# Kernel tuning notes

Measured on AMD Instinct MI355X. Metric: run time of the kernel, lower is better.

## Reference

```python
import jax, jax.numpy as jnp
import numpy as np

NUM_HEAD = 16

def _make_rope(max_len, dim_head, theta=10000.0):
    inv_freq = 1.0 / (theta ** (np.arange(0, dim_head, 2, dtype=np.float32) / dim_head))
    t = np.arange(max_len, dtype=np.float32)
    freqs = np.outer(t, inv_freq)  # [S, dim_head/2]
    return jnp.asarray(np.cos(freqs)), jnp.asarray(np.sin(freqs))

def setup_inputs() -> dict:
    key = jax.random.key(0)
    k1, k2, k3 = jax.random.split(key, 3)
    B, S, D = 2, 2048, 1024
    num_layer = 12
    std = 0.02 / np.sqrt(2 * num_layer)
    x = jax.random.normal(k1, (B, S, D), dtype=jnp.float32)
    wQKV = jax.random.normal(k2, (3 * D, D), dtype=jnp.float32) * std
    wOut = jax.random.normal(k3, (D, D), dtype=jnp.float32) * 0.02
    cos, sin = _make_rope(S, D // NUM_HEAD)
    return {"x": x, "wQKV": wQKV, "wOut": wOut, "cos": cos, "sin": sin}

def _apply_rope(t, cos, sin):
    # t: [B, H, S, dh]; cos/sin: [S, dh/2] -> broadcast [1,1,S,dh/2]
    te, to = t[..., ::2], t[..., 1::2]
    re = te * cos - to * sin
    ro = to * cos + te * sin
    return jnp.stack([re, ro], axis=-1).reshape(t.shape)

def reference(x, wQKV, wOut, cos, sin):
    B, S, D = x.shape
    H = NUM_HEAD
    dh = D // H
    qkv = x @ wQKV.T  # [B, S, 3D]
    q, k, v = jnp.split(qkv, 3, axis=-1)
    q = q.reshape(B, S, H, dh).transpose(0, 2, 1, 3)  # [B,H,S,dh]
    k = k.reshape(B, S, H, dh).transpose(0, 2, 1, 3)
    v = v.reshape(B, S, H, dh).transpose(0, 2, 1, 3)
    c = cos[:S][None, None]
    s = sin[:S][None, None]
    q = _apply_rope(q, c, s)
    k = _apply_rope(k, c, s)
    scores = jnp.einsum('bhsd,bhtd->bhst', q, k) / jnp.sqrt(jnp.asarray(dh, x.dtype))
    causal = jnp.tril(jnp.ones((S, S), dtype=bool))
    scores = jnp.where(causal, scores, jnp.asarray(-jnp.inf, scores.dtype))
    w = jax.nn.softmax(scores, axis=-1)
    out = jnp.einsum('bhst,bhtd->bhsd', w, v)  # [B,H,S,dh]
    out = out.transpose(0, 2, 1, 3).reshape(B, S, D)
    return out @ wOut.T
```

## Files before the change

kernel.cpp:

```cpp
#include <hip/hip_runtime.h>
#include <hip/hip_bf16.h>

typedef __attribute__((ext_vector_type(8))) short bf16x8;
typedef __attribute__((ext_vector_type(4))) short s16x4;
typedef __attribute__((ext_vector_type(4))) float f32x4;

__device__ __forceinline__ short f2bf(float f) {
    unsigned int u = __builtin_bit_cast(unsigned int, f);
    u += 0x7fffu + ((u >> 16) & 1u);
    return (short)(u >> 16);
}

#define GLDS(g, l) __builtin_amdgcn_global_load_lds( \
    (__attribute__((address_space(1))) void*)(g),    \
    (__attribute__((address_space(3))) void*)(l), 16, 0, 0)

#define BARSB() { __builtin_amdgcn_s_barrier(); __builtin_amdgcn_sched_barrier(0); }
#define VMC8()  { asm volatile("s_waitcnt vmcnt(8)" ::: "memory"); __builtin_amdgcn_sched_barrier(0); }
#define VMC7()  { asm volatile("s_waitcnt vmcnt(7)" ::: "memory"); __builtin_amdgcn_sched_barrier(0); }
#define VMC0()  { asm volatile("s_waitcnt vmcnt(0)" ::: "memory"); __builtin_amdgcn_sched_barrier(0); }

__global__ __launch_bounds__(256) void cvt_fused(const float* __restrict__ x,
                                                 const float* __restrict__ wq,
                                                 const float* __restrict__ wo,
                                                 const float* __restrict__ cosT,
                                                 const float* __restrict__ sinT,
                                                 short* __restrict__ xb,
                                                 short* __restrict__ wqb,
                                                 short* __restrict__ wob,
                                                 float2* __restrict__ csT) {
    const int b = blockIdx.x;
    if (b >= 8192) {
        const int idx = (b - 8192) * 256 + threadIdx.x;
        const int i2 = idx >> 11;
        const int s = idx & 2047;
        csT[idx] = make_float2(cosT[s * 32 + i2], sinT[s * 32 + i2]);
        return;
    }
    const float* in; short* out; int i;
    if (b < 4096)      { in = x;  out = xb;  i = b * 256 + threadIdx.x; }
    else if (b < 7168) { in = wq; out = wqb; i = (b - 4096) * 256 + threadIdx.x; }
    else               { in = wo; out = wob; i = (b - 7168) * 256 + threadIdx.x; }
    float4 v = reinterpret_cast<const float4*>(in)[i];
    s16x4 r = { f2bf(v.x), f2bf(v.y), f2bf(v.z), f2bf(v.w) };
    reinterpret_cast<s16x4*>(out)[i] = r;
}

#define LDP 72

__device__ __forceinline__ void load_a(const short* __restrict__ A, int wr, int lo, int hi,
                                       int mh, bf16x8 aF[4][2]) {
#pragma unroll
    for (int mi = 0; mi < 4; ++mi)
#pragma unroll
        for (int kk = 0; kk < 2; ++kk)
            aF[mi][kk] = *reinterpret_cast<const bf16x8*>(
                &A[(wr * 128 + mh * 64 + mi * 16 + lo) * 64 + (((kk * 4 + hi) ^ (lo & 7)) << 3)]);
}
__device__ __forceinline__ void load_b3(const short* __restrict__ B, int wc, int lo, int hi,
                                        bf16x8 bF[3][2]) {
#pragma unroll
    for (int ni = 0; ni < 3; ++ni)
#pragma unroll
        for (int kk = 0; kk < 2; ++kk)
            bF[ni][kk] = *reinterpret_cast<const bf16x8*>(
                &B[(wc * 48 + ni * 16 + lo) * 64 + (((kk * 4 + hi) ^ (lo & 7)) << 3)]);
}
__device__ __forceinline__ void mfma24(const bf16x8 aF[4][2], const bf16x8 bF[3][2],
                                       f32x4 acc[8][3], int mh) {
#pragma unroll
    for (int mi = 0; mi < 4; ++mi)
#pragma unroll
        for (int ni = 0; ni < 3; ++ni)
#pragma unroll
            for (int kk = 0; kk < 2; ++kk)
                acc[mh * 4 + mi][ni] = __builtin_amdgcn_mfma_f32_16x16x32_bf16(
                    aF[mi][kk], bF[ni][kk], acc[mh * 4 + mi][ni], 0, 0, 0);
}

__global__ __launch_bounds__(512, 1) void gemm_qkv_rope(
    const short* __restrict__ X, const short* __restrict__ W,
    const float2* __restrict__ csT,
    short* __restrict__ Qo, short* __restrict__ Ko, short* __restrict__ Vo) {
    __shared__ short ldsA[2][16384];
    __shared__ short ldsB[2][12288];
    const int tid = threadIdx.x;
    const int lane = tid & 63;
    const int w = tid >> 6;
    const int lo = lane & 15, hi = lane >> 4;
    const int wr = w >> 2, wc = w & 3;
    const int lin = blockIdx.x;
    const int xcd = lin & 7;
    const int i_ = lin >> 3;
    const int m0 = ((xcd >> 1) * 4 + (i_ & 3)) * 256;
    const int n0 = ((xcd & 1) * 8 + (i_ >> 2)) * 192;

    f32x4 acc[8][3];
#pragma unroll
    for (int i = 0; i < 8; i++)
#pragma unroll
        for (int j = 0; j < 3; j++) acc[i][j] = {0.f, 0.f, 0.f, 0.f};

    const int srow8 = w * 8 + (lane >> 3);
    const int scx = (((lane & 7) ^ ((lane >> 3) & 7)) << 3);

#define STAGE_A(BUF, KT, IT) GLDS(X + (size_t)(m0 + (IT) * 64 + srow8) * 1024 + ((KT) << 6) + scx, \
                                  (char*)&ldsA[BUF][0] + (IT) * 8192 + w * 1024)
#define STAGE_B(BUF, KT, IT) GLDS(W + (size_t)(n0 + (IT) * 64 + srow8) * 1024 + ((KT) << 6) + scx, \
                                  (char*)&ldsB[BUF][0] + (IT) * 8192 + w * 1024)

    bf16x8 aF[4][2], bF[3][2];

    STAGE_B(0, 0, 0); STAGE_B(0, 0, 1); STAGE_B(0, 0, 2);
    STAGE_A(0, 0, 0); STAGE_A(0, 0, 1); STAGE_A(0, 0, 2); STAGE_A(0, 0, 3);

    for (int t = 0; t < 16; ++t) {
        const int c = t & 1;
        if (t < 15) {
            const int nb_ = c ^ 1, t1 = t + 1;
            STAGE_B(nb_, t1, 0); STAGE_B(nb_, t1, 1); STAGE_B(nb_, t1, 2);
            STAGE_A(nb_, t1, 0); STAGE_A(nb_, t1, 1); STAGE_A(nb_, t1, 2); STAGE_A(nb_, t1, 3);
            VMC7();
        } else {
            VMC0();
        }
        BARSB();
        load_a(&ldsA[c][0], wr, lo, hi, 0, aF);
        load_b3(&ldsB[c][0], wc, lo, hi, bF);
        mfma24(aF, bF, acc, 0);
        load_a(&ldsA[c][0], wr, lo, hi, 1, aF);
        mfma24(aF, bF, acc, 1);
        if (t < 15) BARSB();
    }
#undef STAGE_A
#undef STAGE_B

    const int sfull = m0 + wr * 128 + (hi << 2);
    const int b_ = sfull >> 11;
    const int srow_ = sfull & 2047;
#pragma unroll
    for (int ni = 0; ni < 3; ni++) {
        const int n = n0 + wc * 48 + ni * 16 + lo;
        const int region = n >> 10;
        const int c = n & 1023;
        const int h = c >> 6;
        const int d = c & 63;
        const size_t obase = ((size_t)(b_ * 16 + h) * 2048 + srow_) * 64 + d;
        if (region == 2) {
#pragma unroll
            for (int mi = 0; mi < 8; mi++)
#pragma unroll
                for (int r = 0; r < 4; r++)
                    Vo[obase + (size_t)(mi * 16 + r) * 64] = f2bf(acc[mi][ni][r]);
        } else {
            short* dst = (region == 0) ? Qo : Ko;
            const float scale = (region == 0) ? 0.18033688f : 1.0f;
            const float2* csrow = csT + (size_t)(d >> 1) * 2048 + srow_;
#pragma unroll
            for (int mi = 0; mi < 8; mi++) {
                float4 t0 = *reinterpret_cast<const float4*>(csrow + mi * 16);
                float4 t1 = *reinterpret_cast<const float4*>(csrow + mi * 16 + 2);
                const float cs_[4] = {t0.x, t0.z, t1.x, t1.z};
                const float sn_[4] = {t0.y, t0.w, t1.y, t1.w};
#pragma unroll
                for (int r = 0; r < 4; r++) {
                    float v = acc[mi][ni][r];
                    float other = __shfl_xor(v, 1, 64);
                    float outv = (d & 1) ? (v * cs_[r] + other * sn_[r])
                                         : (v * cs_[r] - other * sn_[r]);
                    dst[obase + (size_t)(mi * 16 + r) * 64] = f2bf(outv * scale);
                }
            }
        }
    }
}

__device__ __forceinline__ void attn_tile_compute(
    const bf16x8 q0, const bf16x8 q1,
    const short* __restrict__ Ks,
    const short (*Vts)[LDP], short* __restrict__ Pw,
    const int lane, const int w, const bool diag,
    float& m_r, float& l_r, f32x4* __restrict__ o_acc) {
    const int lo = lane & 15, hi = lane >> 4;
    const int sx = lo & 7;

    f32x4 sc[4];
#pragma unroll
    for (int nb = 0; nb < 4; nb++) sc[nb] = {0.f, 0.f, 0.f, 0.f};
#pragma unroll
    for (int nb = 0; nb < 4; nb++) {
        const short* kr = &Ks[(nb * 16 + lo) * 64];
        bf16x8 k0 = *reinterpret_cast<const bf16x8*>(&kr[(hi ^ sx) << 3]);
        sc[nb] = __builtin_amdgcn_mfma_f32_16x16x32_bf16(k0, q0, sc[nb], 0, 0, 0);
        bf16x8 k1 = *reinterpret_cast<const bf16x8*>(&kr[((4 + hi) ^ sx) << 3]);
        sc[nb] = __builtin_amdgcn_mfma_f32_16x16x32_bf16(k1, q1, sc[nb], 0, 0, 0);
    }
    if (diag) {
        const int q_ = w * 16 + lo;
        const int kb = (hi << 2);
#pragma unroll
        for (int nb = 0; nb < 4; nb++) {
            const int k_ = nb * 16 + kb;
#pragma unroll
            for (int r = 0; r < 4; r++)
                if (k_ + r > q_) sc[nb][r] = -1e30f;
        }
    }

    float mx = sc[0][0];
#pragma unroll
    for (int nb = 0; nb < 4; nb++)
#pragma unroll
        for (int r = 0; r < 4; r++) mx = fmaxf(mx, sc[nb][r]);
    mx = fmaxf(mx, __shfl_xor(mx, 16, 64));
    mx = fmaxf(mx, __shfl_xor(mx, 32, 64));

    if (!__all(mx <= m_r + 8.0f)) {
        const float mnew = fmaxf(m_r, mx);
        const float alpha = __builtin_amdgcn_exp2f(m_r - mnew);
        m_r = mnew;
        l_r *= alpha;
        float aq[4];
#pragma unroll
        for (int r = 0; r < 4; r++) aq[r] = __shfl(alpha, (hi << 2) + r, 64);
#pragma unroll
        for (int db = 0; db < 4; db++)
#pragma unroll
            for (int r = 0; r < 4; r++) o_acc[db][r] *= aq[r];
    }

    float rs = 0.f;
#pragma unroll
    for (int nb = 0; nb < 4; nb++)
#pragma unroll
        for (int r = 0; r < 4; r++) {
            float e = __builtin_amdgcn_exp2f(sc[nb][r] - m_r);
            sc[nb][r] = e;
            rs += e;
        }
    rs += __shfl_xor(rs, 16, 64);
    rs += __shfl_xor(rs, 32, 64);
    l_r += rs;

    unsigned int* Pw32 = reinterpret_cast<unsigned int*>(Pw);
#pragma unroll
    for (int nb = 0; nb < 4; nb++)
#pragma unroll
        for (int rr = 0; rr < 2; rr++) {
            unsigned int pk;
            asm("v_cvt_pk_bf16_f32 %0, %1, %2"
                : "=v"(pk) : "v"(sc[nb][2 * rr]), "v"(sc[nb][2 * rr + 1]));
            Pw32[lo * (LDP / 2) + nb * 8 + (hi << 1) + rr] = pk;
        }

#pragma unroll
    for (int kk = 0; kk < 2; kk++) {
        bf16x8 pa = *reinterpret_cast<const bf16x8*>(&Pw[lo * LDP + kk * 32 + hi * 8]);
#pragma unroll
        for (int db = 0; db < 4; db++) {
            const int d = db * 16 + lo;
            const int tsw = (kk * 32 + hi * 8) ^ ((((d >> 3) & 7)) << 3);
            bf16x8 vb = *reinterpret_cast<const bf16x8*>(&Vts[d][tsw]);
            o_acc[db] = __builtin_amdgcn_mfma_f32_16x16x32_bf16(pa, vb, o_acc[db], 0, 0, 0);
        }
    }
}

__global__ __launch_bounds__(256) void attn_kernel(
    const short* __restrict__ Q, const short* __restrict__ K,
    const short* __restrict__ V, short* __restrict__ O) {
    __shared__ short Ks[2][64 * 64];
    __shared__ short Vts[2][64][LDP];
    __shared__ short Ps[4][16 * LDP];

    const int tid = threadIdx.x;
    const int lane = tid & 63;
    const int w = tid >> 6;
    const int lo = lane & 15, hi = lane >> 4;
    const int sx = lo & 7;
    const int lin = blockIdx.x;
    const int bh = lin & 31;
    const int qt = 31 - (lin >> 5);
    const int b_ = bh >> 4, h = bh & 15;
    const size_t base = (size_t)bh * 2048 * 64;

    const int krow = tid >> 2;
    const int cq = (tid & 3) * 2;
    const int ksw = krow & 7;

    bf16x8 q0, q1;
    {
        const short* src = Q + base + (size_t)(qt * 64 + krow) * 64 + cq * 8;
        bf16x8 a = *reinterpret_cast<const bf16x8*>(src);
        bf16x8 b = *reinterpret_cast<const bf16x8*>(src + 8);
        *reinterpret_cast<bf16x8*>(&Ks[0][krow * 64 + ((cq ^ ksw) << 3)]) = a;
        *reinterpret_cast<bf16x8*>(&Ks[0][krow * 64 + (((cq + 1) ^ ksw) << 3)]) = b;
        __syncthreads();
        q0 = *reinterpret_cast<const bf16x8*>(&Ks[0][(w * 16 + lo) * 64 + ((hi ^ sx) << 3)]);
        q1 = *reinterpret_cast<const bf16x8*>(&Ks[0][(w * 16 + lo) * 64 + (((4 + hi) ^ sx) << 3)]);
        __syncthreads();
    }

    float m_r = -1e30f, l_r = 0.f;
    f32x4 o_acc[4];
#pragma unroll
    for (int db = 0; db < 4; db++) o_acc[db] = {0.f, 0.f, 0.f, 0.f};

    const int u2 = tid >> 3;
    const int vdb8 = (tid & 7) * 8;
    const int vswz = (tid & 7) << 3;
    const int tw = (2 * u2) ^ vswz;

    bf16x8 kr0, kr1, vr0, vr1;
    kr0 = *reinterpret_cast<const bf16x8*>(K + base + (size_t)krow * 64 + cq * 8);
    kr1 = *reinterpret_cast<const bf16x8*>(K + base + (size_t)krow * 64 + cq * 8 + 8);
    vr0 = *reinterpret_cast<const bf16x8*>(V + base + (size_t)(2 * u2) * 64 + vdb8);
    vr1 = *reinterpret_cast<const bf16x8*>(V + base + (size_t)(2 * u2 + 1) * 64 + vdb8);

    int c = 0;
    for (int j = 0; j <= qt; j++) {
        *reinterpret_cast<bf16x8*>(&Ks[c][krow * 64 + ((cq ^ ksw) << 3)]) = kr0;
        *reinterpret_cast<bf16x8*>(&Ks[c][krow * 64 + (((cq + 1) ^ ksw) << 3)]) = kr1;
#pragma unroll
        for (int i = 0; i < 8; i++) {
            unsigned int pv = (unsigned int)(unsigned short)vr0[i] |
                              ((unsigned int)(unsigned short)vr1[i] << 16);
            *reinterpret_cast<unsigned int*>(&Vts[c][vdb8 + i][tw]) = pv;
        }
        __syncthreads();
        if (j < qt) {
            const size_t jb2 = (size_t)(j + 1) * 64;
            kr0 = *reinterpret_cast<const bf16x8*>(K + base + (jb2 + krow) * 64 + cq * 8);
            kr1 = *reinterpret_cast<const bf16x8*>(K + base + (jb2 + krow) * 64 + cq * 8 + 8);
            vr0 = *reinterpret_cast<const bf16x8*>(V + base + (jb2 + 2 * u2) * 64 + vdb8);
            vr1 = *reinterpret_cast<const bf16x8*>(V + base + (jb2 + 2 * u2 + 1) * 64 + vdb8);
        }

        attn_tile_compute(q0, q1, Ks[c], Vts[c], &Ps[w][0], lane, w, j == qt, m_r, l_r, o_acc);
        c ^= 1;
    }

    float inv[4];
#pragma unroll
    for (int r = 0; r < 4; r++) inv[r] = 1.f / __shfl(l_r, (hi << 2) + r, 64);

    short* Op = O + ((size_t)b_ * 2048) * 1024 + (size_t)h * 64;
#pragma unroll
    for (int r = 0; r < 4; r++) {
        const int row = qt * 64 + w * 16 + (hi << 2) + r;
#pragma unroll
        for (int db = 0; db < 4; db++)
            Op[(size_t)row * 1024 + db * 16 + lo] = f2bf(o_acc[db][r] * inv[r]);
    }
}

__global__ __launch_bounds__(256) void gemm_out(
    const short* __restrict__ A, const short* __restrict__ W,
    float* __restrict__ C) {
    __shared__ short As[2][128 * 64];
    __shared__ short Bs[2][128 * 64];
    const int tid = threadIdx.x;
    const int lane = tid & 63;
    const int w = tid >> 6;
    const int lo = lane & 15, hi = lane >> 4;
    const int wr = w >> 1, wc = w & 1;
    const int lin = blockIdx.x;
    const int wg = (lin & 7) * 32 + (lin >> 3);
    const int n0 = (wg & 7) * 128;
    const int m0 = (wg >> 3) * 128;
    const int K = 1024;

    f32x4 acc[4][4];
#pragma unroll
    for (int i = 0; i < 4; i++)
#pragma unroll
        for (int j = 0; j < 4; j++) acc[i][j] = {0.f, 0.f, 0.f, 0.f};

    const int srow = w * 8 + (lane >> 3);
    const int scx = (((lane & 7) ^ ((lane >> 3) & 7)) << 3);
    const short* gA = A + (size_t)(m0 + srow) * K + scx;
    const short* gB = W + (size_t)(n0 + srow) * K + scx;

#pragma unroll
    for (int it = 0; it < 4; it++)
        GLDS(gA + (size_t)it * 32 * K, (char*)As[0] + it * 4096 + w * 1024);
#pragma unroll
    for (int it = 0; it < 4; it++)
        GLDS(gB + (size_t)it * 32 * K, (char*)Bs[0] + it * 4096 + w * 1024);

    for (int t = 0; t < 16; t++) {
        const int c = t & 1;
        if (t < 15) {
            const int k1 = (t + 1) * 64;
#pragma unroll
            for (int it = 0; it < 4; it++)
                GLDS(gA + k1 + (size_t)it * 32 * K, (char*)As[c ^ 1] + it * 4096 + w * 1024);
#pragma unroll
            for (int it = 0; it < 4; it++)
                GLDS(gB + k1 + (size_t)it * 32 * K, (char*)Bs[c ^ 1] + it * 4096 + w * 1024);
            VMC8();
        } else {
            VMC0();
        }
        BARSB();
#pragma unroll
        for (int kk = 0; kk < 2; kk++) {
            bf16x8 a[4], b[4];
#pragma unroll
            for (int mi = 0; mi < 4; mi++)
                a[mi] = *reinterpret_cast<const bf16x8*>(
                    &As[c][(wr * 64 + mi * 16 + lo) * 64 + (((kk * 4 + hi) ^ (lo & 7)) << 3)]);
#pragma unroll
            for (int ni = 0; ni < 4; ni++)
                b[ni] = *reinterpret_cast<const bf16x8*>(
                    &Bs[c][(wc * 64 + ni * 16 + lo) * 64 + (((kk * 4 + hi) ^ (lo & 7)) << 3)]);
#pragma unroll
            for (int mi = 0; mi < 4; mi++)
#pragma unroll
                for (int ni = 0; ni < 4; ni++)
                    acc[mi][ni] = __builtin_amdgcn_mfma_f32_16x16x32_bf16(
                        a[mi], b[ni], acc[mi][ni], 0, 0, 0);
        }
        if (t < 15) BARSB();
    }

#pragma unroll
    for (int mi = 0; mi < 4; mi++) {
#pragma unroll
        for (int r = 0; r < 4; r++) {
            const int m = m0 + wr * 64 + mi * 16 + (hi << 2) + r;
#pragma unroll
            for (int ni = 0; ni < 4; ni++) {
                const int n = n0 + wc * 64 + ni * 16 + lo;
                C[(size_t)m * 1024 + n] = acc[mi][ni][r];
            }
        }
    }
}

extern "C" void kernel_launch(void* const* d_in, const int* in_sizes, int n_in,
                              void* d_out, int out_size, void* d_ws, size_t ws_size,
                              hipStream_t stream) {
    const float* x = (const float*)d_in[0];
    const float* wQKV = (const float*)d_in[1];
    const float* wOut = (const float*)d_in[2];
    const float* cosT = (const float*)d_in[3];
    const float* sinT = (const float*)d_in[4];
    float* out = (float*)d_out;

    char* ws = (char*)d_ws;
    const size_t MB = 1024 * 1024;
    short* xb    = (short*)(ws);
    short* wqkvb = (short*)(ws + 8 * MB);
    short* woutb = (short*)(ws + 14 * MB);
    short* Qbuf  = (short*)(ws + 16 * MB);
    short* Kbuf  = (short*)(ws + 24 * MB);
    short* Vbuf  = (short*)(ws + 32 * MB);
    short* Obuf  = (short*)(ws + 40 * MB);
    float2* csT  = (float2*)(ws + 48 * MB);

    cvt_fused<<<8448, 256, 0, stream>>>(x, wQKV, wOut, cosT, sinT, xb, wqkvb, woutb, csT);
    gemm_qkv_rope<<<256, 512, 0, stream>>>(xb, wqkvb, csT, Qbuf, Kbuf, Vbuf);
    attn_kernel<<<1024, 256, 0, stream>>>(Qbuf, Kbuf, Vbuf, Obuf);
    gemm_out<<<256, 256, 0, stream>>>(Obuf, woutb, out);
}
```

Baseline: 108.2 us.

## Enlarge attention query tile to 128 rows with 8 waves sharing K/V tiles

The attention kernel now handles 128 query rows per block with 512 threads (8 waves), so each K/V tile loaded into shared memory serves twice as many query rows and global K/V traffic is halved. The grid shrinks to 512 blocks. Per-wave causal masking now uses a per-wave offset, and waves skip tiles that lie entirely above their diagonal. The cost is fewer, larger blocks, which means worse load balance across the causal triangle, some idle waves on the last tiles, and heavier barrier synchronisation.

```diff
diff --git a/kernel.cpp b/kernel.cpp
--- a/kernel.cpp
+++ b/kernel.cpp
@@ -179,7 +179,7 @@
     const bf16x8 q0, const bf16x8 q1,
     const short* __restrict__ Ks,
     const short (*Vts)[LDP], short* __restrict__ Pw,
-    const int lane, const int w, const bool diag,
+    const int lane, const bool diag, const int kq,
     float& m_r, float& l_r, f32x4* __restrict__ o_acc) {
     const int lo = lane & 15, hi = lane >> 4;
     const int sx = lo & 7;
@@ -196,14 +196,13 @@
         sc[nb] = __builtin_amdgcn_mfma_f32_16x16x32_bf16(k1, q1, sc[nb], 0, 0, 0);
     }
     if (diag) {
-        const int q_ = w * 16 + lo;
         const int kb = (hi << 2);
 #pragma unroll
         for (int nb = 0; nb < 4; nb++) {
             const int k_ = nb * 16 + kb;
 #pragma unroll
             for (int r = 0; r < 4; r++)
-                if (k_ + r > q_) sc[nb][r] = -1e30f;
+                if (k_ + r > kq) sc[nb][r] = -1e30f;
         }
     }
 
@@ -266,12 +265,12 @@
     }
 }
 
-__global__ __launch_bounds__(256) void attn_kernel(
+__global__ __launch_bounds__(512) void attn_kernel(
     const short* __restrict__ Q, const short* __restrict__ K,
     const short* __restrict__ V, short* __restrict__ O) {
     __shared__ short Ks[2][64 * 64];
     __shared__ short Vts[2][64][LDP];
-    __shared__ short Ps[4][16 * LDP];
+    __shared__ short Ps[8][16 * LDP];
 
     const int tid = threadIdx.x;
     const int lane = tid & 63;
@@ -280,25 +279,32 @@
     const int sx = lo & 7;
     const int lin = blockIdx.x;
     const int bh = lin & 31;
-    const int qt = 31 - (lin >> 5);
+    const int qb = 15 - (lin >> 5);
     const int b_ = bh >> 4, h = bh & 15;
     const size_t base = (size_t)bh * 2048 * 64;
-
-    const int krow = tid >> 2;
-    const int cq = (tid & 3) * 2;
+    const int q0row = qb * 128;
+
+    const int krow = tid >> 3;
+    const int cq = tid & 7;
     const int ksw = krow & 7;
 
     bf16x8 q0, q1;
     {
-        const short* src = Q + base + (size_t)(qt * 64 + krow) * 64 + cq * 8;
-        bf16x8 a = *reinterpret_cast<const bf16x8*>(src);
-        bf16x8 b = *reinterpret_cast<const bf16x8*>(src + 8);
-        *reinterpret_cast<bf16x8*>(&Ks[0][krow * 64 + ((cq ^ ksw) << 3)]) = a;
-        *reinterpret_cast<bf16x8*>(&Ks[0][krow * 64 + (((cq + 1) ^ ksw) << 3)]) = b;
-        __syncthreads();
-        q0 = *reinterpret_cast<const bf16x8*>(&Ks[0][(w * 16 + lo) * 64 + ((hi ^ sx) << 3)]);
-        q1 = *reinterpret_cast<const bf16x8*>(&Ks[0][(w * 16 + lo) * 64 + (((4 + hi) ^ sx) << 3)]);
-        __syncthreads();
+        const int wl = w & 3;
+#pragma unroll
+        for (int round = 0; round < 2; round++) {
+            const short* src = Q + base + (size_t)(q0row + round * 64 + krow) * 64 + cq * 8;
+            *reinterpret_cast<bf16x8*>(&Ks[0][krow * 64 + ((cq ^ ksw) << 3)]) =
+                *reinterpret_cast<const bf16x8*>(src);
+            __syncthreads();
+            if ((w >> 2) == round) {
+                q0 = *reinterpret_cast<const bf16x8*>(
+                    &Ks[0][(wl * 16 + lo) * 64 + ((hi ^ sx) << 3)]);
+                q1 = *reinterpret_cast<const bf16x8*>(
+                    &Ks[0][(wl * 16 + lo) * 64 + (((4 + hi) ^ sx) << 3)]);
+            }
+            __syncthreads();
+        }
     }
 
     float m_r = -1e30f, l_r = 0.f;
@@ -306,37 +312,39 @@
 #pragma unroll
     for (int db = 0; db < 4; db++) o_acc[db] = {0.f, 0.f, 0.f, 0.f};
 
-    const int u2 = tid >> 3;
-    const int vdb8 = (tid & 7) * 8;
-    const int vswz = (tid & 7) << 3;
+    const int u2 = tid >> 4;
+    const int vdb4 = (tid & 15) * 4;
+    const int vswz = ((vdb4 >> 3) & 7) << 3;
     const int tw = (2 * u2) ^ vswz;
 
-    bf16x8 kr0, kr1, vr0, vr1;
-    kr0 = *reinterpret_cast<const bf16x8*>(K + base + (size_t)krow * 64 + cq * 8);
-    kr1 = *reinterpret_cast<const bf16x8*>(K + base + (size_t)krow * 64 + cq * 8 + 8);
-    vr0 = *reinterpret_cast<const bf16x8*>(V + base + (size_t)(2 * u2) * 64 + vdb8);
-    vr1 = *reinterpret_cast<const bf16x8*>(V + base + (size_t)(2 * u2 + 1) * 64 + vdb8);
-
+    bf16x8 kr;
+    s16x4 vr0, vr1;
+    kr = *reinterpret_cast<const bf16x8*>(K + base + (size_t)krow * 64 + cq * 8);
+    vr0 = *reinterpret_cast<const s16x4*>(V + base + (size_t)(2 * u2) * 64 + vdb4);
+    vr1 = *reinterpret_cast<const s16x4*>(V + base + (size_t)(2 * u2 + 1) * 64 + vdb4);
+
+    const int jmax = 2 * qb + 1;
     int c = 0;
-    for (int j = 0; j <= qt; j++) {
-        *reinterpret_cast<bf16x8*>(&Ks[c][krow * 64 + ((cq ^ ksw) << 3)]) = kr0;
-        *reinterpret_cast<bf16x8*>(&Ks[c][krow * 64 + (((cq + 1) ^ ksw) << 3)]) = kr1;
-#pragma unroll
-        for (int i = 0; i < 8; i++) {
+    for (int j = 0; j <= jmax; j++) {
+        *reinterpret_cast<bf16x8*>(&Ks[c][krow * 64 + ((cq ^ ksw) << 3)]) = kr;
+#pragma unroll
+        for (int i = 0; i < 4; i++) {
             unsigned int pv = (unsigned int)(unsigned short)vr0[i] |
                               ((unsigned int)(unsigned short)vr1[i] << 16);
-            *reinterpret_cast<unsigned int*>(&Vts[c][vdb8 + i][tw]) = pv;
+            *reinterpret_cast<unsigned int*>(&Vts[c][vdb4 + i][tw]) = pv;
         }
         __syncthreads();
-        if (j < qt) {
+        if (j < jmax) {
             const size_t jb2 = (size_t)(j + 1) * 64;
-            kr0 = *reinterpret_cast<const bf16x8*>(K + base + (jb2 + krow) * 64 + cq * 8);
-            kr1 = *reinterpret_cast<const bf16x8*>(K + base + (jb2 + krow) * 64 + cq * 8 + 8);
-            vr0 = *reinterpret_cast<const bf16x8*>(V + base + (jb2 + 2 * u2) * 64 + vdb8);
-            vr1 = *reinterpret_cast<const bf16x8*>(V + base + (jb2 + 2 * u2 + 1) * 64 + vdb8);
-        }
-
-        attn_tile_compute(q0, q1, Ks[c], Vts[c], &Ps[w][0], lane, w, j == qt, m_r, l_r, o_acc);
+            kr = *reinterpret_cast<const bf16x8*>(K + base + (jb2 + krow) * 64 + cq * 8);
+            vr0 = *reinterpret_cast<const s16x4*>(V + base + (jb2 + 2 * u2) * 64 + vdb4);
+            vr1 = *reinterpret_cast<const s16x4*>(V + base + (jb2 + 2 * u2 + 1) * 64 + vdb4);
+        }
+        const int kqw = q0row + w * 16 - j * 64;
+        if (kqw >= 0) {
+            attn_tile_compute(q0, q1, Ks[c], Vts[c], &Ps[w][0], lane,
+                              kqw < 63, kqw + lo, m_r, l_r, o_acc);
+        }
         c ^= 1;
     }
 
@@ -347,7 +355,7 @@
     short* Op = O + ((size_t)b_ * 2048) * 1024 + (size_t)h * 64;
 #pragma unroll
     for (int r = 0; r < 4; r++) {
-        const int row = qt * 64 + w * 16 + (hi << 2) + r;
+        const int row = q0row + w * 16 + (hi << 2) + r;
 #pragma unroll
         for (int db = 0; db < 4; db++)
             Op[(size_t)row * 1024 + db * 16 + lo] = f2bf(o_acc[db][r] * inv[r]);
@@ -461,6 +469,6 @@
 
     cvt_fused<<<8448, 256, 0, stream>>>(x, wQKV, wOut, cosT, sinT, xb, wqkvb, woutb, csT);
     gemm_qkv_rope<<<256, 512, 0, stream>>>(xb, wqkvb, csT, Qbuf, Kbuf, Vbuf);
-    attn_kernel<<<1024, 256, 0, stream>>>(Qbuf, Kbuf, Vbuf, Obuf);
+    attn_kernel<<<512, 512, 0, stream>>>(Qbuf, Kbuf, Vbuf, Obuf);
     gemm_out<<<256, 256, 0, stream>>>(Obuf, woutb, out);
 }
```

New measurement: 112.5 us. 1.04x slower.
